# Performance work log

Measured on AMD Instinct MI355X. Metric: run time of the kernel, lower is better.

The kernel has to match this reference:

```python
import jax, jax.numpy as jnp
import numpy as np

HIDDEN = 256
NUM_NODES = 262144
NUM_GRAPHS = 4096
CHUNK_SIZE = 32  # hard-coded in the torch forward
NUM_CHUNKS = NUM_GRAPHS // CHUNK_SIZE


def setup_inputs() -> dict:
    key = jax.random.key(0)
    k1, k2, k3, k4 = jax.random.split(key, 4)
    x = jax.random.normal(k1, (NUM_NODES, HIDDEN), dtype=jnp.float32)
    # sorted graph ids covering all graphs 0..NUM_GRAPHS-1 (PyG batch vector)
    batch = (jnp.arange(NUM_NODES, dtype=jnp.int64) * NUM_GRAPHS) // NUM_NODES
    # attention MLP params: Linear(H,H) -> Tanh -> Linear(H,1, bias=False)
    s1 = 1.0 / np.sqrt(HIDDEN)
    W1 = jax.random.uniform(k2, (HIDDEN, HIDDEN), jnp.float32, -s1, s1)
    b1 = jax.random.uniform(k3, (HIDDEN,), jnp.float32, -s1, s1)
    W2 = jax.random.uniform(k4, (HIDDEN, 1), jnp.float32, -s1, s1)
    return {"x": x, "batch": batch, "W1": W1, "b1": b1, "W2": W2}


def reference(x, batch, W1, b1, W2):
    # attention scores: Linear -> Tanh -> Linear (no bias)  [N]
    scores = (jnp.tanh(x @ W1 + b1) @ W2)[:, 0]
    # softmax is over ALL nodes within each chunk of 32 consecutive graphs
    chunk_id = batch // CHUNK_SIZE
    m = jax.ops.segment_max(scores, chunk_id, num_segments=NUM_CHUNKS)
    e = jnp.exp(scores - m[chunk_id])
    denom = jax.ops.segment_sum(e, chunk_id, num_segments=NUM_CHUNKS)
    w = e / denom[chunk_id]  # [N]
    # global_add_pool of (w * x) per graph  -> [NUM_GRAPHS, HIDDEN]
    out = jax.ops.segment_sum(w[:, None] * x, batch, num_segments=NUM_GRAPHS)
    return out
```

## Files before the change

### kernel.cpp

```cpp
#include <hip/hip_runtime.h>

#define NODES 262144
#define HID 256
#define GRAPHS 4096
#define SROWS 64
#define TPB 8
#define NHALF (NODES / 32)
#define NSUP (NODES / SROWS)

typedef __attribute__((ext_vector_type(8))) short short8;
typedef __attribute__((ext_vector_type(4))) float floatx4;

__device__ __forceinline__ short bf16_rne(float f) {
  union { float f; unsigned int u; } v; v.f = f;
  unsigned int u = v.u;
  u += 0x7fffu + ((u >> 16) & 1u);
  return (short)(u >> 16);
}

__device__ __forceinline__ unsigned int cvt_pk_bf16(float lo, float hi) {
  unsigned int r;
  asm("v_cvt_pk_bf16_f32 %0, %1, %2" : "=v"(r) : "v"(lo), "v"(hi));
  return r;
}

__device__ __forceinline__ float bf16_to_f32(unsigned short u) {
  union { unsigned int u; float f; } v;
  v.u = ((unsigned int)u) << 16;
  return v.f;
}

__device__ __forceinline__ float fast_tanh(float x) {
  float e = exp2f(x * 2.885390082f);
  return 1.0f - 2.0f * __builtin_amdgcn_rcpf(e + 1.0f);
}

__global__ __launch_bounds__(256) void k_prep(const float* __restrict__ w1,
                                              short* __restrict__ w1t) {
  __shared__ short t[64][65];
  const int bk = (blockIdx.x & 3) * 64;
  const int bn = (blockIdx.x >> 2) * 64;
  const int tx = threadIdx.x & 63, ty = threadIdx.x >> 6;
#pragma unroll
  for (int i = 0; i < 64; i += 4)
    t[tx][ty + i] = bf16_rne(w1[(bk + ty + i) * HID + bn + tx]);
  __syncthreads();
#pragma unroll
  for (int i = 0; i < 64; i += 4)
    w1t[(bn + ty + i) * HID + bk + tx] = t[ty + i][tx];
}

__global__ __launch_bounds__(512, 2) void k_fused(
    const float* __restrict__ x, const short* __restrict__ w1t,
    const float* __restrict__ b1, const float* __restrict__ w2,
    float* __restrict__ Ah, float* __restrict__ mh, float* __restrict__ lh)
{
  __shared__ short As[SROWS * 264];
  __shared__ float part[8][SROWS];
  __shared__ float wbuf[SROWS];
  const int tid = threadIdx.x;
  const int wave = tid >> 6, lane = tid & 63;
  const int quad = lane >> 4, l15 = lane & 15;

  short8 bfrag[8][2];
  {
    const short* bbase = w1t + (wave * 32 + l15) * HID + quad * 8;
#pragma unroll
    for (int kk = 0; kk < 8; ++kk)
#pragma unroll
      for (int ct = 0; ct < 2; ++ct)
        bfrag[kk][ct] = *(const short8*)(bbase + ct * 16 * HID + kk * 32);
  }

  float b1v[2], w2v[2];
#pragma unroll
  for (int ct = 0; ct < 2; ++ct) {
    int n = wave * 32 + ct * 16 + l15;
    b1v[ct] = b1[n];
    w2v[ct] = w2[n];
  }

  const short* abase = &As[l15 * 264 + quad * 8];

  const int sup0 = blockIdx.x * TPB;

  float4 r[8];
  {
    const float4* xin = ((const float4*)x) + (size_t)sup0 * (SROWS * 64);
#pragma unroll
    for (int i = 0; i < 8; ++i) r[i] = xin[tid + i * 512];
  }

  for (int tt = 0; tt < TPB; ++tt) {
    __syncthreads();

#pragma unroll
    for (int i = 0; i < 8; ++i) {
      int f = tid + i * 512;
      int row = f >> 6, c4 = f & 63;
      uint2 p;
      p.x = cvt_pk_bf16(r[i].x, r[i].y);
      p.y = cvt_pk_bf16(r[i].z, r[i].w);
      *(uint2*)&As[row * 264 + c4 * 4] = p;
    }
    __syncthreads();

    if (tt + 1 < TPB) {
      const float4* xin =
          ((const float4*)x) + (size_t)(sup0 + tt + 1) * (SROWS * 64);
#pragma unroll
      for (int i = 0; i < 8; ++i) r[i] = xin[tid + i * 512];
    }

    floatx4 acc[4][2];
#pragma unroll
    for (int rt = 0; rt < 4; ++rt)
#pragma unroll
      for (int ct = 0; ct < 2; ++ct)
#pragma unroll
        for (int e = 0; e < 4; ++e) acc[rt][ct][e] = 0.f;

#pragma unroll
    for (int kk = 0; kk < 8; ++kk) {
      short8 afrag[4];
#pragma unroll
      for (int rt = 0; rt < 4; ++rt)
        afrag[rt] = *(const short8*)(abase + rt * 16 * 264 + kk * 32);
#pragma unroll
      for (int rt = 0; rt < 4; ++rt)
#pragma unroll
        for (int ct = 0; ct < 2; ++ct)
          acc[rt][ct] = __builtin_amdgcn_mfma_f32_16x16x32_bf16(
              afrag[rt], bfrag[kk][ct], acc[rt][ct], 0, 0, 0);
    }

    float sc[4][4];
#pragma unroll
    for (int rt = 0; rt < 4; ++rt)
#pragma unroll
      for (int reg = 0; reg < 4; ++reg) {
        float s = 0.f;
#pragma unroll
        for (int ct = 0; ct < 2; ++ct)
          s += fast_tanh(acc[rt][ct][reg] + b1v[ct]) * w2v[ct];
        sc[rt][reg] = s;
      }
#pragma unroll
    for (int mask = 1; mask <= 8; mask <<= 1)
#pragma unroll
      for (int rt = 0; rt < 4; ++rt)
#pragma unroll
        for (int reg = 0; reg < 4; ++reg)
          sc[rt][reg] += __shfl_xor(sc[rt][reg], mask, 64);
    if (l15 == 0) {
#pragma unroll
      for (int rt = 0; rt < 4; ++rt)
#pragma unroll
        for (int reg = 0; reg < 4; ++reg)
          part[wave][rt * 16 + quad * 4 + reg] = sc[rt][reg];
    }
    __syncthreads();

    if (wave < 2 && lane < 32) {
      int row = wave * 32 + lane;
      float s = 0.f;
#pragma unroll
      for (int w = 0; w < 8; ++w) s += part[w][row];
      float m = s;
#pragma unroll
      for (int mask = 1; mask < 32; mask <<= 1)
        m = fmaxf(m, __shfl_xor(m, mask, 32));
      float e = __expf(s - m);
      float l = e;
#pragma unroll
      for (int mask = 1; mask < 32; mask <<= 1)
        l += __shfl_xor(l, mask, 32);
      wbuf[row] = e;
      if (lane == 0) {
        int h = 2 * (sup0 + tt) + wave;
        mh[h] = m; lh[h] = l;
      }
    }
    __syncthreads();

    {
      const int halfsel = tid >> 8, col = tid & 255;
      const int rbase = halfsel * 32;
      float pacc = 0.f;
#pragma unroll
      for (int j = 0; j < 8; ++j) {
        float4 wv = *(const float4*)&wbuf[rbase + j * 4];
#pragma unroll
        for (int q = 0; q < 4; ++q) {
          int i = rbase + j * 4 + q;
          unsigned short u = *(const unsigned short*)&As[i * 264 + col];
          float wq = (q == 0) ? wv.x : (q == 1) ? wv.y : (q == 2) ? wv.z : wv.w;
          pacc = fmaf(wq, bf16_to_f32(u), pacc);
        }
      }
      Ah[(size_t)(2 * (sup0 + tt) + halfsel) * HID + col] = pacc;
    }
  }
}

__global__ __launch_bounds__(256) void k_finish(
    const float* __restrict__ Ah, const float* __restrict__ mh,
    const float* __restrict__ lh, float* __restrict__ out)
{
  const int c = blockIdx.x, t = threadIdx.x;
  __shared__ float sm[64], sl[64], sh[64];
  if (t < 64) { sm[t] = mh[c * 64 + t]; sl[t] = lh[c * 64 + t]; }
  __syncthreads();
  float m = sm[0];
#pragma unroll 8
  for (int j = 1; j < 64; ++j) m = fmaxf(m, sm[j]);
  float den = 0.f;
#pragma unroll 8
  for (int j = 0; j < 64; ++j) den += sl[j] * __expf(sm[j] - m);
  float inv = 1.0f / den;
  if (t < 64) sh[t] = __expf(sm[t] - m) * inv;
  __syncthreads();
  const float* ab = Ah + (size_t)c * 64 * HID;
#pragma unroll 4
  for (int j = 0; j < 32; ++j) {
    float v = ab[(2 * j) * HID + t] * sh[2 * j] +
              ab[(2 * j + 1) * HID + t] * sh[2 * j + 1];
    out[((size_t)c * 32 + j) * HID + t] = v;
  }
}

extern "C" void kernel_launch(void* const* d_in, const int* in_sizes, int n_in,
                              void* d_out, int out_size, void* d_ws, size_t ws_size,
                              hipStream_t stream) {
  const float* x  = (const float*)d_in[0];
  const float* w1 = (const float*)d_in[2];
  const float* b1 = (const float*)d_in[3];
  const float* w2 = (const float*)d_in[4];
  float* out = (float*)d_out;

  char* ws = (char*)d_ws;
  float* Ah  = (float*)ws;
  float* mhb = (float*)(ws + (NHALF * HID) * 4);
  float* lhb = mhb + NHALF;
  short* w1t = (short*)(ws + (NHALF * HID + 2 * NHALF) * 4);

  k_prep  <<<16, 256, 0, stream>>>(w1, w1t);
  k_fused <<<NSUP / TPB, 512, 0, stream>>>(x, w1t, b1, w2, Ah, mhb, lhb);
  k_finish<<<GRAPHS / 32, 256, 0, stream>>>(Ah, mhb, lhb, out);
}
```

Baseline: 384.2 us.

## Double-buffer x tile loads two tiles ahead and split finish kernel across more blocks

The fused kernel now holds two register buffers of x tiles, so each tile's global load is issued two iterations before it is used, giving more latency hiding behind the MFMA and softmax work. Each thread loads two adjacent float4s and writes a single 16-byte LDS store instead of two 8-byte ones. The finish kernel is split four ways per chunk, giving 512 blocks instead of 128, which raises parallelism for the final reduction. The cost is higher register pressure (16 float4 buffers), which could cause spills under the 512x2 launch bound.

```diff
diff --git a/kernel.cpp b/kernel.cpp
--- a/kernel.cpp
+++ b/kernel.cpp
@@ -49,6 +49,101 @@
   for (int i = 0; i < 64; i += 4)
     w1t[(bn + ty + i) * HID + bk + tx] = t[ty + i][tx];
 }
+
+
+#define ISSUE(R, T)                                                          \
+  do {                                                                       \
+    const float4* xin_ =                                                     \
+        ((const float4*)x) + (size_t)(sup0 + (T)) * (SROWS * 64);            \
+    _Pragma("unroll") for (int i_ = 0; i_ < 4; ++i_) {                       \
+      R[2 * i_]     = xin_[2 * tid + i_ * 1024];                             \
+      R[2 * i_ + 1] = xin_[2 * tid + i_ * 1024 + 1];                         \
+    }                                                                        \
+  } while (0)
+
+#define COMMIT(R)                                                            \
+  do {                                                                       \
+    _Pragma("unroll") for (int i_ = 0; i_ < 4; ++i_) {                       \
+      int f_ = 2 * tid + i_ * 1024;                                          \
+      int row_ = f_ >> 6, c4_ = f_ & 63;                                     \
+      uint4 p_;                                                              \
+      p_.x = cvt_pk_bf16(R[2 * i_].x, R[2 * i_].y);                          \
+      p_.y = cvt_pk_bf16(R[2 * i_].z, R[2 * i_].w);                          \
+      p_.z = cvt_pk_bf16(R[2 * i_ + 1].x, R[2 * i_ + 1].y);                  \
+      p_.w = cvt_pk_bf16(R[2 * i_ + 1].z, R[2 * i_ + 1].w);                  \
+      *(uint4*)&As[row_ * 264 + c4_ * 4] = p_;                               \
+    }                                                                        \
+  } while (0)
+
+#define COMPUTE(T)                                                           \
+  do {                                                                       \
+    floatx4 acc[4][2];                                                       \
+    _Pragma("unroll") for (int rt = 0; rt < 4; ++rt)                         \
+        _Pragma("unroll") for (int ct = 0; ct < 2; ++ct)                     \
+            _Pragma("unroll") for (int e = 0; e < 4; ++e) acc[rt][ct][e] = 0.f; \
+    _Pragma("unroll") for (int kk = 0; kk < 8; ++kk) {                       \
+      short8 afrag[4];                                                       \
+      _Pragma("unroll") for (int rt = 0; rt < 4; ++rt)                       \
+          afrag[rt] = *(const short8*)(abase + rt * 16 * 264 + kk * 32);     \
+      _Pragma("unroll") for (int rt = 0; rt < 4; ++rt)                       \
+          _Pragma("unroll") for (int ct = 0; ct < 2; ++ct)                   \
+              acc[rt][ct] = __builtin_amdgcn_mfma_f32_16x16x32_bf16(         \
+                  afrag[rt], bfrag[kk][ct], acc[rt][ct], 0, 0, 0);           \
+    }                                                                        \
+    float sc[4][4];                                                          \
+    _Pragma("unroll") for (int rt = 0; rt < 4; ++rt)                         \
+        _Pragma("unroll") for (int reg = 0; reg < 4; ++reg) {                \
+      float s_ = 0.f;                                                        \
+      _Pragma("unroll") for (int ct = 0; ct < 2; ++ct)                       \
+          s_ += fast_tanh(acc[rt][ct][reg] + b1v[ct]) * w2v[ct];             \
+      sc[rt][reg] = s_;                                                      \
+    }                                                                        \
+    _Pragma("unroll") for (int mask = 1; mask <= 8; mask <<= 1)              \
+        _Pragma("unroll") for (int rt = 0; rt < 4; ++rt)                     \
+            _Pragma("unroll") for (int reg = 0; reg < 4; ++reg)              \
+                sc[rt][reg] += __shfl_xor(sc[rt][reg], mask, 64);            \
+    if (l15 == 0) {                                                          \
+      _Pragma("unroll") for (int rt = 0; rt < 4; ++rt)                       \
+          _Pragma("unroll") for (int reg = 0; reg < 4; ++reg)                \
+              part[wave][rt * 16 + quad * 4 + reg] = sc[rt][reg];            \
+    }                                                                        \
+    __syncthreads();                                   \
+    if (wave < 2 && lane < 32) {                                             \
+      int row_ = wave * 32 + lane;                                           \
+      float s_ = 0.f;                                                        \
+      _Pragma("unroll") for (int w_ = 0; w_ < 8; ++w_) s_ += part[w_][row_]; \
+      float m_ = s_;                                                         \
+      _Pragma("unroll") for (int mask = 1; mask < 32; mask <<= 1)            \
+          m_ = fmaxf(m_, __shfl_xor(m_, mask, 32));                          \
+      float e_ = __expf(s_ - m_);                                            \
+      float l_ = e_;                                                         \
+      _Pragma("unroll") for (int mask = 1; mask < 32; mask <<= 1)            \
+          l_ += __shfl_xor(l_, mask, 32);                                    \
+      wbuf[row_] = e_;                                                       \
+      if (lane == 0) {                                                       \
+        int h_ = 2 * (sup0 + (T)) + wave;                                    \
+        mh[h_] = m_; lh[h_] = l_;                                            \
+      }                                                                      \
+    }                                                                        \
+    __syncthreads();                                   \
+    {                                                                        \
+      const int halfsel_ = tid >> 8, col_ = tid & 255;                       \
+      const int rbase_ = halfsel_ * 32;                                      \
+      float pacc_ = 0.f;                                                     \
+      _Pragma("unroll") for (int j_ = 0; j_ < 8; ++j_) {                     \
+        float4 wv_ = *(const float4*)&wbuf[rbase_ + j_ * 4];                 \
+        _Pragma("unroll") for (int q_ = 0; q_ < 4; ++q_) {                   \
+          int i_ = rbase_ + j_ * 4 + q_;                                     \
+          unsigned short u_ = *(const unsigned short*)&As[i_ * 264 + col_];  \
+          float wq_ = (q_ == 0) ? wv_.x                                      \
+                    : (q_ == 1) ? wv_.y                                      \
+                    : (q_ == 2) ? wv_.z : wv_.w;                             \
+          pacc_ = fmaf(wq_, bf16_to_f32(u_), pacc_);                         \
+        }                                                                    \
+      }                                                                      \
+      Ah[(size_t)(2 * (sup0 + (T)) + halfsel_) * HID + col_] = pacc_;        \
+    }                                                                        \
+  } while (0)
 
 __global__ __launch_bounds__(512, 2) void k_fused(
     const float* __restrict__ x, const short* __restrict__ w1t,
@@ -84,122 +179,25 @@
 
   const int sup0 = blockIdx.x * TPB;
 
-  float4 r[8];
-  {
-    const float4* xin = ((const float4*)x) + (size_t)sup0 * (SROWS * 64);
-#pragma unroll
-    for (int i = 0; i < 8; ++i) r[i] = xin[tid + i * 512];
-  }
-
-  for (int tt = 0; tt < TPB; ++tt) {
-    __syncthreads();
-
-#pragma unroll
-    for (int i = 0; i < 8; ++i) {
-      int f = tid + i * 512;
-      int row = f >> 6, c4 = f & 63;
-      uint2 p;
-      p.x = cvt_pk_bf16(r[i].x, r[i].y);
-      p.y = cvt_pk_bf16(r[i].z, r[i].w);
-      *(uint2*)&As[row * 264 + c4 * 4] = p;
-    }
-    __syncthreads();
-
-    if (tt + 1 < TPB) {
-      const float4* xin =
-          ((const float4*)x) + (size_t)(sup0 + tt + 1) * (SROWS * 64);
-#pragma unroll
-      for (int i = 0; i < 8; ++i) r[i] = xin[tid + i * 512];
-    }
-
-    floatx4 acc[4][2];
-#pragma unroll
-    for (int rt = 0; rt < 4; ++rt)
-#pragma unroll
-      for (int ct = 0; ct < 2; ++ct)
-#pragma unroll
-        for (int e = 0; e < 4; ++e) acc[rt][ct][e] = 0.f;
-
-#pragma unroll
-    for (int kk = 0; kk < 8; ++kk) {
-      short8 afrag[4];
-#pragma unroll
-      for (int rt = 0; rt < 4; ++rt)
-        afrag[rt] = *(const short8*)(abase + rt * 16 * 264 + kk * 32);
-#pragma unroll
-      for (int rt = 0; rt < 4; ++rt)
-#pragma unroll
-        for (int ct = 0; ct < 2; ++ct)
-          acc[rt][ct] = __builtin_amdgcn_mfma_f32_16x16x32_bf16(
-              afrag[rt], bfrag[kk][ct], acc[rt][ct], 0, 0, 0);
-    }
-
-    float sc[4][4];
-#pragma unroll
-    for (int rt = 0; rt < 4; ++rt)
-#pragma unroll
-      for (int reg = 0; reg < 4; ++reg) {
-        float s = 0.f;
-#pragma unroll
-        for (int ct = 0; ct < 2; ++ct)
-          s += fast_tanh(acc[rt][ct][reg] + b1v[ct]) * w2v[ct];
-        sc[rt][reg] = s;
-      }
-#pragma unroll
-    for (int mask = 1; mask <= 8; mask <<= 1)
-#pragma unroll
-      for (int rt = 0; rt < 4; ++rt)
-#pragma unroll
-        for (int reg = 0; reg < 4; ++reg)
-          sc[rt][reg] += __shfl_xor(sc[rt][reg], mask, 64);
-    if (l15 == 0) {
-#pragma unroll
-      for (int rt = 0; rt < 4; ++rt)
-#pragma unroll
-        for (int reg = 0; reg < 4; ++reg)
-          part[wave][rt * 16 + quad * 4 + reg] = sc[rt][reg];
-    }
-    __syncthreads();
-
-    if (wave < 2 && lane < 32) {
-      int row = wave * 32 + lane;
-      float s = 0.f;
-#pragma unroll
-      for (int w = 0; w < 8; ++w) s += part[w][row];
-      float m = s;
-#pragma unroll
-      for (int mask = 1; mask < 32; mask <<= 1)
-        m = fmaxf(m, __shfl_xor(m, mask, 32));
-      float e = __expf(s - m);
-      float l = e;
-#pragma unroll
-      for (int mask = 1; mask < 32; mask <<= 1)
-        l += __shfl_xor(l, mask, 32);
-      wbuf[row] = e;
-      if (lane == 0) {
-        int h = 2 * (sup0 + tt) + wave;
-        mh[h] = m; lh[h] = l;
-      }
-    }
-    __syncthreads();
-
-    {
-      const int halfsel = tid >> 8, col = tid & 255;
-      const int rbase = halfsel * 32;
-      float pacc = 0.f;
-#pragma unroll
-      for (int j = 0; j < 8; ++j) {
-        float4 wv = *(const float4*)&wbuf[rbase + j * 4];
-#pragma unroll
-        for (int q = 0; q < 4; ++q) {
-          int i = rbase + j * 4 + q;
-          unsigned short u = *(const unsigned short*)&As[i * 264 + col];
-          float wq = (q == 0) ? wv.x : (q == 1) ? wv.y : (q == 2) ? wv.z : wv.w;
-          pacc = fmaf(wq, bf16_to_f32(u), pacc);
-        }
-      }
-      Ah[(size_t)(2 * (sup0 + tt) + halfsel) * HID + col] = pacc;
-    }
+  float4 rA[8], rB[8];
+  ISSUE(rA, 0);
+  ISSUE(rB, 1);
+
+#pragma unroll 1
+  for (int it = 0; it < TPB / 2; ++it) {
+    const int t0 = 2 * it, t1 = 2 * it + 1;
+
+    __syncthreads();
+    COMMIT(rA);
+    __syncthreads();
+    if (t0 + 2 < TPB) ISSUE(rA, t0 + 2);
+    COMPUTE(t0);
+
+    __syncthreads();
+    COMMIT(rB);
+    __syncthreads();
+    if (t1 + 2 < TPB) ISSUE(rB, t1 + 2);
+    COMPUTE(t1);
   }
 }
 
@@ -207,7 +205,7 @@
     const float* __restrict__ Ah, const float* __restrict__ mh,
     const float* __restrict__ lh, float* __restrict__ out)
 {
-  const int c = blockIdx.x, t = threadIdx.x;
+  const int c = blockIdx.x >> 2, q = blockIdx.x & 3, t = threadIdx.x;
   __shared__ float sm[64], sl[64], sh[64];
   if (t < 64) { sm[t] = mh[c * 64 + t]; sl[t] = lh[c * 64 + t]; }
   __syncthreads();
@@ -221,8 +219,9 @@
   if (t < 64) sh[t] = __expf(sm[t] - m) * inv;
   __syncthreads();
   const float* ab = Ah + (size_t)c * 64 * HID;
-#pragma unroll 4
-  for (int j = 0; j < 32; ++j) {
+#pragma unroll
+  for (int jj = 0; jj < 8; ++jj) {
+    int j = q * 8 + jj;
     float v = ab[(2 * j) * HID + t] * sh[2 * j] +
               ab[(2 * j + 1) * HID + t] * sh[2 * j + 1];
     out[((size_t)c * 32 + j) * HID + t] = v;
@@ -246,5 +245,5 @@
 
   k_prep  <<<16, 256, 0, stream>>>(w1, w1t);
   k_fused <<<NSUP / TPB, 512, 0, stream>>>(x, w1t, b1, w2, Ah, mhb, lhb);
-  k_finish<<<GRAPHS / 32, 256, 0, stream>>>(Ah, mhb, lhb, out);
-}
+  k_finish<<<GRAPHS / 8, 256, 0, stream>>>(Ah, mhb, lhb, out);
+}
```

Measured after the change: 392.6 us. 1.02x slower.
